# Kernel optimization log

Measured on AMD Instinct MI355X. Metric: run time of the kernel, lower is better.

The kernel has to match this reference:

```python
import jax, jax.numpy as jnp
import numpy as np

D_MODEL = 1024
NUM_HEADS = 16
D_K = D_MODEL // NUM_HEADS


def setup_inputs() -> dict:
    key = jax.random.key(0)
    ks = jax.random.split(key, 9)
    s = 1.0 / np.sqrt(D_MODEL)
    x = jax.random.normal(ks[0], (4, 2048, D_MODEL), dtype=jnp.float32)
    Wq = jax.random.uniform(ks[1], (D_MODEL, D_MODEL), jnp.float32, -s, s)
    bq = jax.random.uniform(ks[2], (D_MODEL,), jnp.float32, -s, s)
    Wk = jax.random.uniform(ks[3], (D_MODEL, D_MODEL), jnp.float32, -s, s)
    bk = jax.random.uniform(ks[4], (D_MODEL,), jnp.float32, -s, s)
    Wv = jax.random.uniform(ks[5], (D_MODEL, D_MODEL), jnp.float32, -s, s)
    bv = jax.random.uniform(ks[6], (D_MODEL,), jnp.float32, -s, s)
    Wo = jax.random.uniform(ks[7], (D_MODEL, D_MODEL), jnp.float32, -s, s)
    bo = jax.random.uniform(ks[8], (D_MODEL,), jnp.float32, -s, s)
    return {"x": x, "Wq": Wq, "bq": bq, "Wk": Wk, "bk": bk,
            "Wv": Wv, "bv": bv, "Wo": Wo, "bo": bo}


def reference(x, Wq, bq, Wk, bk, Wv, bv, Wo, bo):
    B, S, _ = x.shape
    # project and split heads: [B,S,D] -> [B,H,S,dk]
    def heads(W, b):
        return (x @ W + b).reshape(B, S, NUM_HEADS, D_K).transpose(0, 2, 1, 3)
    q = heads(Wq, bq)
    k = heads(Wk, bk)
    v = heads(Wv, bv)
    scores = jnp.einsum('bhqd,bhkd->bhqk', q, k) / jnp.sqrt(jnp.float32(D_K))
    attn = jax.nn.softmax(scores, axis=-1)
    out = jnp.einsum('bhqk,bhkd->bhqd', attn, v)
    out = out.transpose(0, 2, 1, 3).reshape(B, S, D_MODEL)
    return out @ Wo + bo
```

## Files before the change

kernel.cpp:

```cpp
#include <hip/hip_runtime.h>
#include <hip/hip_bf16.h>

#define D_MODEL 1024
#define NUM_HEADS 16
#define D_K 64
#define B_SZ 4
#define SEQ 2048
#define SCALE_Q 0.180336881f

typedef short bf16x8 __attribute__((ext_vector_type(8)));
typedef float f32x4 __attribute__((ext_vector_type(4)));
typedef unsigned short u16;

__device__ __forceinline__ unsigned cvtpk(float a, float b) {
    unsigned r;
    asm("v_cvt_pk_bf16_f32 %0, %1, %2" : "=v"(r) : "v"(a), "v"(b));
    return r;
}
__device__ __forceinline__ u16 f2bf(float f) {
    return (u16)cvtpk(f, f);
}
__device__ __forceinline__ float exp2a(float x) {
    float r;
    asm("v_exp_f32 %0, %1" : "=v"(r) : "v"(x));
    return r;
}
__device__ __forceinline__ void gload_lds16(const u16* g, u16* l) {
    __builtin_amdgcn_global_load_lds(
        (const __attribute__((address_space(1))) unsigned int*)g,
        (__attribute__((address_space(3))) unsigned int*)l, 16, 0, 0);
}

__global__ __launch_bounds__(256) void prep_all(
    const float* __restrict__ xin, u16* __restrict__ xbf,
    const float* __restrict__ W0, const float* __restrict__ W1,
    const float* __restrict__ W2, const float* __restrict__ W3,
    u16* __restrict__ Wt)
{
    __shared__ float tile[64][65];
    const int t = threadIdx.x;
    if (blockIdx.x < 1024) {
        const int n8 = (B_SZ * SEQ * D_MODEL) / 8;
        for (int i = blockIdx.x * 256 + t; i < n8; i += 1024 * 256) {
            float4 a = ((const float4*)xin)[(size_t)i * 2];
            float4 b = ((const float4*)xin)[(size_t)i * 2 + 1];
            uint4 o;
            o.x = cvtpk(a.x, a.y);
            o.y = cvtpk(a.z, a.w);
            o.z = cvtpk(b.x, b.y);
            o.w = cvtpk(b.z, b.w);
            const int j = i ^ ((i >> 7) & 7);
            ((uint4*)xbf)[j] = o;
        }
        return;
    }
    const int id = blockIdx.x - 1024;
    const int z  = id >> 8;
    const int by = (id >> 4) & 15;
    const int bx = id & 15;
    const float* W = z == 0 ? W0 : z == 1 ? W1 : z == 2 ? W2 : W3;
    u16* out = Wt + (size_t)z * D_MODEL * D_MODEL;
    const int k0 = by * 64;
    const int n0 = bx * 64;
    #pragma unroll
    for (int it = 0; it < 4; ++it) {
        int idx = it * 256 + t;
        int r = idx >> 4;
        int c = (idx & 15) * 4;
        float4 v = *(const float4*)(W + (size_t)(k0 + r) * D_MODEL + n0 + c);
        tile[r][c + 0] = v.x; tile[r][c + 1] = v.y;
        tile[r][c + 2] = v.z; tile[r][c + 3] = v.w;
    }
    __syncthreads();
    #pragma unroll
    for (int it = 0; it < 2; ++it) {
        int idx = it * 256 + t;
        int r = idx >> 3;
        int c = (idx & 7) * 8;
        uint4 o;
        o.x = cvtpk(tile[c + 0][r], tile[c + 1][r]);
        o.y = cvtpk(tile[c + 2][r], tile[c + 3][r]);
        o.z = cvtpk(tile[c + 4][r], tile[c + 5][r]);
        o.w = cvtpk(tile[c + 6][r], tile[c + 7][r]);
        const int csw = (((idx & 7) ^ (r & 7)) * 8);
        *(uint4*)(out + (size_t)(n0 + r) * D_MODEL + k0 + csw) = o;
    }
}

__global__ __launch_bounds__(512) void gemm_qkv(
    const u16* __restrict__ A, const u16* __restrict__ Wt,
    const float* __restrict__ bq, const float* __restrict__ bk,
    const float* __restrict__ bv, u16* __restrict__ Yb)
{
    __shared__ u16 As[2][128][64];
    __shared__ u16 Bs[2][128][64];
    const int t    = threadIdx.x;
    const int lane = t & 63;
    const int wid  = t >> 6;
    const int wm   = wid >> 2;
    const int wn   = wid & 3;
    const int g    = lane >> 4;
    const int lr   = lane & 15;
    const int m0   = blockIdx.y * 128;
    const int n0   = blockIdx.x * 128;
    const int K    = D_MODEL;
    const int xm   = (lr & 7) << 3;

    const int srow8 = lane >> 3;
    const int scol  = (lane & 7) * 8;

    f32x4 acc[4][2];
    #pragma unroll
    for (int i = 0; i < 4; ++i)
        #pragma unroll
        for (int j = 0; j < 2; ++j)
            acc[i][j] = (f32x4){0.f, 0.f, 0.f, 0.f};

    #pragma unroll
    for (int it = 0; it < 2; ++it) {
        const int seg = it * 8 + wid;
        gload_lds16(A  + (size_t)(m0 + seg * 8 + srow8) * K + scol, &As[0][seg * 8][0]);
        gload_lds16(Wt + (size_t)(n0 + seg * 8 + srow8) * K + scol, &Bs[0][seg * 8][0]);
    }
    __syncthreads();

    for (int k0 = 0; k0 < K; k0 += 64) {
        const int cur = (k0 >> 6) & 1;
        if (k0 + 64 < K) {
            const int nb = cur ^ 1;
            #pragma unroll
            for (int it = 0; it < 2; ++it) {
                const int seg = it * 8 + wid;
                gload_lds16(A  + (size_t)(m0 + seg * 8 + srow8) * K + k0 + 64 + scol, &As[nb][seg * 8][0]);
                gload_lds16(Wt + (size_t)(n0 + seg * 8 + srow8) * K + k0 + 64 + scol, &Bs[nb][seg * 8][0]);
            }
        }
        #pragma unroll
        for (int s = 0; s < 2; ++s) {
            bf16x8 af[4], bfr[2];
            #pragma unroll
            for (int mt = 0; mt < 4; ++mt)
                af[mt] = *(const bf16x8*)(&As[cur][wm * 64 + mt * 16 + lr][(g * 8 + s * 32) ^ xm]);
            #pragma unroll
            for (int nt = 0; nt < 2; ++nt)
                bfr[nt] = *(const bf16x8*)(&Bs[cur][wn * 32 + nt * 16 + lr][(g * 8 + s * 32) ^ xm]);
            #pragma unroll
            for (int mt = 0; mt < 4; ++mt)
                #pragma unroll
                for (int nt = 0; nt < 2; ++nt)
                    acc[mt][nt] = __builtin_amdgcn_mfma_f32_16x16x32_bf16(
                        af[mt], bfr[nt], acc[mt][nt], 0, 0, 0);
        }
        __syncthreads();
    }

    const int which = n0 >> 10;
    const float scale = (which == 0) ? SCALE_Q : 1.0f;
    const float* bp = (which == 0) ? bq : (which == 1) ? bk : bv;
    u16* dst = Yb + (size_t)which * ((size_t)B_SZ * SEQ * D_MODEL);

    float bv2[2];
    #pragma unroll
    for (int nt = 0; nt < 2; ++nt)
        bv2[nt] = bp[((n0 + wn * 32 + nt * 16 + lr) & 1023)];

    #pragma unroll
    for (int mt = 0; mt < 4; ++mt) {
        #pragma unroll
        for (int nt = 0; nt < 2; ++nt) {
            float v4[4];
            #pragma unroll
            for (int r = 0; r < 4; ++r) v4[r] = (acc[mt][nt][r] + bv2[nt]) * scale;
            const int mbase = m0 + wm * 64 + mt * 16 + g * 4;
            const int nn = (n0 + wn * 32 + nt * 16 + lr) & 1023;
            const int h = nn >> 6, d = nn & 63;
            const int bb = mbase >> 11, s2 = mbase & 2047;
            if (which == 2) {
                const int z  = s2 & 63;
                const int zp = (z & 32) + 8 * ((z & 15) >> 2) + 4 * ((z >> 4) & 1);
                const int col = zp ^ ((d & 7) << 3);
                uint2 o;
                o.x = cvtpk(v4[0], v4[1]);
                o.y = cvtpk(v4[2], v4[3]);
                *(uint2*)&dst[(((size_t)(bb * NUM_HEADS + h) * D_K + d) * SEQ) + (s2 & ~63) + col] = o;
            } else {
                #pragma unroll
                for (int r = 0; r < 4; ++r) {
                    const int s2r = s2 + r;
                    const int dd = (which == 1) ? (d ^ ((s2r & 7) << 3)) : d;
                    dst[(((size_t)(bb * NUM_HEADS + h) * SEQ) + s2r) * D_K + dd] = f2bf(v4[r]);
                }
            }
        }
    }
}

__global__ __launch_bounds__(512) void gemm_o(
    const u16* __restrict__ A, const u16* __restrict__ Wt,
    const float* __restrict__ bias, float* __restrict__ Y)
{
    __shared__ u16 As[2][128][64];
    __shared__ u16 Bs[2][128][64];
    const int t    = threadIdx.x;
    const int lane = t & 63;
    const int wid  = t >> 6;
    const int wm   = wid >> 2;
    const int wn   = wid & 3;
    const int g    = lane >> 4;
    const int lr   = lane & 15;
    const int m0   = blockIdx.y * 128;
    const int n0   = blockIdx.x * 128;
    const int K    = D_MODEL;
    const int xm   = (lr & 7) << 3;

    const int srow8 = lane >> 3;
    const int scol  = (lane & 7) * 8;

    f32x4 acc[4][2];
    #pragma unroll
    for (int i = 0; i < 4; ++i)
        #pragma unroll
        for (int j = 0; j < 2; ++j)
            acc[i][j] = (f32x4){0.f, 0.f, 0.f, 0.f};

    #pragma unroll
    for (int it = 0; it < 2; ++it) {
        const int seg = it * 8 + wid;
        gload_lds16(A  + (size_t)(m0 + seg * 8 + srow8) * K + scol, &As[0][seg * 8][0]);
        gload_lds16(Wt + (size_t)(n0 + seg * 8 + srow8) * K + scol, &Bs[0][seg * 8][0]);
    }
    __syncthreads();

    for (int k0 = 0; k0 < K; k0 += 64) {
        const int cur = (k0 >> 6) & 1;
        if (k0 + 64 < K) {
            const int nb = cur ^ 1;
            #pragma unroll
            for (int it = 0; it < 2; ++it) {
                const int seg = it * 8 + wid;
                gload_lds16(A  + (size_t)(m0 + seg * 8 + srow8) * K + k0 + 64 + scol, &As[nb][seg * 8][0]);
                gload_lds16(Wt + (size_t)(n0 + seg * 8 + srow8) * K + k0 + 64 + scol, &Bs[nb][seg * 8][0]);
            }
        }
        #pragma unroll
        for (int s = 0; s < 2; ++s) {
            bf16x8 af[4], bfr[2];
            #pragma unroll
            for (int mt = 0; mt < 4; ++mt)
                af[mt] = *(const bf16x8*)(&As[cur][wm * 64 + mt * 16 + lr][(g * 8 + s * 32) ^ xm]);
            #pragma unroll
            for (int nt = 0; nt < 2; ++nt)
                bfr[nt] = *(const bf16x8*)(&Bs[cur][wn * 32 + nt * 16 + lr][(g * 8 + s * 32) ^ xm]);
            #pragma unroll
            for (int mt = 0; mt < 4; ++mt)
                #pragma unroll
                for (int nt = 0; nt < 2; ++nt)
                    acc[mt][nt] = __builtin_amdgcn_mfma_f32_16x16x32_bf16(
                        af[mt], bfr[nt], acc[mt][nt], 0, 0, 0);
        }
        __syncthreads();
    }

    float bv2[2];
    #pragma unroll
    for (int nt = 0; nt < 2; ++nt) bv2[nt] = bias[n0 + wn * 32 + nt * 16 + lr];

    #pragma unroll
    for (int mt = 0; mt < 4; ++mt)
        #pragma unroll
        for (int nt = 0; nt < 2; ++nt)
            #pragma unroll
            for (int r = 0; r < 4; ++r) {
                const int m = m0 + wm * 64 + mt * 16 + g * 4 + r;
                const int n = n0 + wn * 32 + nt * 16 + lr;
                Y[(size_t)m * D_MODEL + n] = acc[mt][nt][r] + bv2[nt];
            }
}

__global__ __launch_bounds__(512, 4) void attn_mfma(
    const u16* __restrict__ Q, const u16* __restrict__ Kb,
    const u16* __restrict__ Vt, u16* __restrict__ ctx)
{
    __shared__ u16 Ks[2][128][64];
    __shared__ u16 Vs[2][64][128];
    const int t    = threadIdx.x;
    const int lane = t & 63;
    const int w    = t >> 6;
    const int g    = lane >> 4;
    const int lr   = lane & 15;
    const int fid  = blockIdx.x + (blockIdx.y << 3) + (blockIdx.z << 7);
    const int oid  = (fid & 7) * 64 + (fid >> 3);
    const int qt   = oid & 7;
    const int h    = (oid >> 3) & 15;
    const int b    = oid >> 7;
    const size_t hoff = ((size_t)b * NUM_HEADS + h) * SEQ * D_K;

    bf16x8 qf[2][2];
    #pragma unroll
    for (int u = 0; u < 2; ++u) {
        const int q = qt * 256 + w * 32 + u * 16 + lr;
        qf[u][0] = *(const bf16x8*)(Q + hoff + (size_t)q * D_K + g * 8);
        qf[u][1] = *(const bf16x8*)(Q + hoff + (size_t)q * D_K + g * 8 + 32);
    }

    bf16x8 onesf;
    #pragma unroll
    for (int j = 0; j < 8; ++j) onesf[j] = (short)0x3F80;

    const int krow = w * 16 + (lane >> 3);
    const int kcol = (lane & 7) * 8;
    const u16* ksrc = Kb + hoff + (size_t)krow * D_K + kcol;
    const int vrow = w * 8 + (lane >> 4);
    const int vcol = (lane & 15) * 8;
    const u16* vsrc = Vt + hoff + (size_t)vrow * SEQ + vcol;

    const int xm = (lr & 7) << 3;

    f32x4 acc_o[2][4];
    f32x4 acc_l[2];
    #pragma unroll
    for (int u = 0; u < 2; ++u) {
        acc_l[u] = (f32x4){0.f, 0.f, 0.f, 0.f};
        #pragma unroll
        for (int n = 0; n < 4; ++n) acc_o[u][n] = (f32x4){0.f, 0.f, 0.f, 0.f};
    }

    gload_lds16(ksrc,               &Ks[0][w * 16][0]);
    gload_lds16(ksrc + 8 * D_K,     &Ks[0][w * 16 + 8][0]);
    gload_lds16(vsrc,               &Vs[0][w * 8][0]);
    gload_lds16(vsrc + 4 * SEQ,     &Vs[0][w * 8 + 4][0]);

    int bu = 0;
    for (int kt = 0; kt < SEQ / 128; ++kt) {
        __syncthreads();
        if (kt + 1 < SEQ / 128) {
            const size_t kv0 = (size_t)(kt + 1) * 128;
            const int nb = bu ^ 1;
            gload_lds16(ksrc + kv0 * D_K,       &Ks[nb][w * 16][0]);
            gload_lds16(ksrc + (kv0 + 8) * D_K, &Ks[nb][w * 16 + 8][0]);
            gload_lds16(vsrc + kv0,             &Vs[nb][w * 8][0]);
            gload_lds16(vsrc + 4 * SEQ + kv0,   &Vs[nb][w * 8 + 4][0]);
        }

        #pragma unroll
        for (int hv = 0; hv < 2; ++hv) {
            f32x4 sc[2][4];
            #pragma unroll
            for (int u = 0; u < 2; ++u)
                #pragma unroll
                for (int mt = 0; mt < 4; ++mt) sc[u][mt] = (f32x4){0.f, 0.f, 0.f, 0.f};
            __builtin_amdgcn_s_setprio(1);
            #pragma unroll
            for (int s = 0; s < 2; ++s)
                #pragma unroll
                for (int mt = 0; mt < 4; ++mt) {
                    bf16x8 kf = *(const bf16x8*)(
                        &Ks[bu][hv * 64 + mt * 16 + lr][(g * 8 + s * 32) ^ xm]);
                    sc[0][mt] = __builtin_amdgcn_mfma_f32_16x16x32_bf16(kf, qf[0][s], sc[0][mt], 0, 0, 0);
                    sc[1][mt] = __builtin_amdgcn_mfma_f32_16x16x32_bf16(kf, qf[1][s], sc[1][mt], 0, 0, 0);
                }
            __builtin_amdgcn_s_setprio(0);

            union { bf16x8 v; unsigned u[4]; } pa[2][2];
            #pragma unroll
            for (int u = 0; u < 2; ++u) {
                #pragma unroll
                for (int mt = 0; mt < 4; ++mt)
                    #pragma unroll
                    for (int r = 0; r < 4; ++r)
                        sc[u][mt][r] = exp2a(sc[u][mt][r]);
                #pragma unroll
                for (int s = 0; s < 2; ++s) {
                    pa[u][s].u[0] = cvtpk(sc[u][2 * s][0],     sc[u][2 * s][1]);
                    pa[u][s].u[1] = cvtpk(sc[u][2 * s][2],     sc[u][2 * s][3]);
                    pa[u][s].u[2] = cvtpk(sc[u][2 * s + 1][0], sc[u][2 * s + 1][1]);
                    pa[u][s].u[3] = cvtpk(sc[u][2 * s + 1][2], sc[u][2 * s + 1][3]);
                }
            }

            __builtin_amdgcn_s_setprio(1);
            #pragma unroll
            for (int s = 0; s < 2; ++s) {
                #pragma unroll
                for (int n = 0; n < 4; ++n) {
                    bf16x8 vf = *(const bf16x8*)(
                        &Vs[bu][16 * n + lr][hv * 64 + ((32 * s + 8 * g) ^ xm)]);
                    acc_o[0][n] = __builtin_amdgcn_mfma_f32_16x16x32_bf16(pa[0][s].v, vf, acc_o[0][n], 0, 0, 0);
                    acc_o[1][n] = __builtin_amdgcn_mfma_f32_16x16x32_bf16(pa[1][s].v, vf, acc_o[1][n], 0, 0, 0);
                }
                acc_l[0] = __builtin_amdgcn_mfma_f32_16x16x32_bf16(pa[0][s].v, onesf, acc_l[0], 0, 0, 0);
                acc_l[1] = __builtin_amdgcn_mfma_f32_16x16x32_bf16(pa[1][s].v, onesf, acc_l[1], 0, 0, 0);
            }
            __builtin_amdgcn_s_setprio(0);
        }
        bu ^= 1;
    }

    #pragma unroll
    for (int u = 0; u < 2; ++u) {
        f32x4 linv;
        #pragma unroll
        for (int r = 0; r < 4; ++r) linv[r] = 1.0f / acc_l[u][r];
        #pragma unroll
        for (int n = 0; n < 4; ++n)
            #pragma unroll
            for (int r = 0; r < 4; ++r) {
                const int qrow = qt * 256 + w * 32 + u * 16 + 4 * g + r;
                const int col  = (h * D_K + 16 * n + lr) ^ ((qrow & 7) << 3);
                ctx[((size_t)b * SEQ + qrow) * D_MODEL + col] =
                    f2bf(acc_o[u][n][r] * linv[r]);
            }
    }
}

extern "C" void kernel_launch(void* const* d_in, const int* in_sizes, int n_in,
                              void* d_out, int out_size, void* d_ws, size_t ws_size,
                              hipStream_t stream)
{
    const float* x  = (const float*)d_in[0];
    const float* Wq = (const float*)d_in[1];
    const float* bq = (const float*)d_in[2];
    const float* Wk = (const float*)d_in[3];
    const float* bk = (const float*)d_in[4];
    const float* Wv = (const float*)d_in[5];
    const float* bv = (const float*)d_in[6];
    const float* Wo = (const float*)d_in[7];
    const float* bo = (const float*)d_in[8];
    float* out = (float*)d_out;

    char* ws = (char*)d_ws;
    const size_t MB = 1024 * 1024;
    u16* xbf  = (u16*)(ws);
    u16* Wt   = (u16*)(ws + 16 * MB);
    u16* Qbf  = (u16*)(ws + 24 * MB);
    u16* ctxb = (u16*)(ws + 72 * MB);
    u16* Kbf  = Qbf + (size_t)B_SZ * SEQ * D_MODEL;
    u16* Vtw  = Kbf + (size_t)B_SZ * SEQ * D_MODEL;

    prep_all<<<2048, 256, 0, stream>>>(x, xbf, Wq, Wk, Wv, Wo, Wt);

    gemm_qkv<<<dim3(3 * D_MODEL / 128, (B_SZ * SEQ) / 128), 512, 0, stream>>>(
        xbf, Wt, bq, bk, bv, Qbf);

    attn_mfma<<<dim3(SEQ / 256, NUM_HEADS, B_SZ), 512, 0, stream>>>(Qbf, Kbf, Vtw, ctxb);

    gemm_o<<<dim3(D_MODEL / 128, (B_SZ * SEQ) / 128), 512, 0, stream>>>(
        ctxb, Wt + 3 * (size_t)D_MODEL * D_MODEL, bo, out);
}
```

Before: 163.4 us.

## Triple-buffer GEMM K-loop with 32-wide tiles, vmcnt waits and new swizzle

New measurement: 171.2 us. 4.8% more time.

```diff
diff --git a/kernel.cpp b/kernel.cpp
--- a/kernel.cpp
+++ b/kernel.cpp
@@ -49,7 +49,7 @@
             o.y = cvtpk(a.z, a.w);
             o.z = cvtpk(b.x, b.y);
             o.w = cvtpk(b.z, b.w);
-            const int j = i ^ ((i >> 7) & 7);
+            const int j = (i & ~3) | ((i ^ (i >> 9)) & 3);
             ((uint4*)xbf)[j] = o;
         }
         return;
@@ -75,25 +75,26 @@
     #pragma unroll
     for (int it = 0; it < 2; ++it) {
         int idx = it * 256 + t;
-        int r = idx >> 3;
-        int c = (idx & 7) * 8;
+        int r  = idx >> 3;
+        int cI = idx & 7;
+        int c  = cI * 8;
         uint4 o;
         o.x = cvtpk(tile[c + 0][r], tile[c + 1][r]);
         o.y = cvtpk(tile[c + 2][r], tile[c + 3][r]);
         o.z = cvtpk(tile[c + 4][r], tile[c + 5][r]);
         o.w = cvtpk(tile[c + 6][r], tile[c + 7][r]);
-        const int csw = (((idx & 7) ^ (r & 7)) * 8);
-        *(uint4*)(out + (size_t)(n0 + r) * D_MODEL + k0 + csw) = o;
-    }
-}
-
-__global__ __launch_bounds__(512) void gemm_qkv(
+        const int cs = (cI & ~3) | ((cI ^ (r >> 2)) & 3);
+        *(uint4*)(out + (size_t)(n0 + r) * D_MODEL + k0 + cs * 8) = o;
+    }
+}
+
+__global__ __launch_bounds__(512, 4) void gemm_qkv(
     const u16* __restrict__ A, const u16* __restrict__ Wt,
     const float* __restrict__ bq, const float* __restrict__ bk,
     const float* __restrict__ bv, u16* __restrict__ Yb)
 {
-    __shared__ u16 As[2][128][64];
-    __shared__ u16 Bs[2][128][64];
+    __shared__ u16 As[3][128][32];
+    __shared__ u16 Bs[3][128][32];
     const int t    = threadIdx.x;
     const int lane = t & 63;
     const int wid  = t >> 6;
@@ -101,13 +102,13 @@
     const int wn   = wid & 3;
     const int g    = lane >> 4;
     const int lr   = lane & 15;
+    const int xc   = (lr >> 2) & 3;
     const int m0   = blockIdx.y * 128;
     const int n0   = blockIdx.x * 128;
     const int K    = D_MODEL;
-    const int xm   = (lr & 7) << 3;
-
-    const int srow8 = lane >> 3;
-    const int scol  = (lane & 7) * 8;
+
+    const u16* Asrc = A  + (size_t)(m0 + wid * 16 + (lane >> 2)) * K + (lane & 3) * 8;
+    const u16* Bsrc = Wt + (size_t)(n0 + wid * 16 + (lane >> 2)) * K + (lane & 3) * 8;
 
     f32x4 acc[4][2];
     #pragma unroll
@@ -116,42 +117,36 @@
         for (int j = 0; j < 2; ++j)
             acc[i][j] = (f32x4){0.f, 0.f, 0.f, 0.f};
 
-    #pragma unroll
-    for (int it = 0; it < 2; ++it) {
-        const int seg = it * 8 + wid;
-        gload_lds16(A  + (size_t)(m0 + seg * 8 + srow8) * K + scol, &As[0][seg * 8][0]);
-        gload_lds16(Wt + (size_t)(n0 + seg * 8 + srow8) * K + scol, &Bs[0][seg * 8][0]);
-    }
-    __syncthreads();
-
-    for (int k0 = 0; k0 < K; k0 += 64) {
-        const int cur = (k0 >> 6) & 1;
-        if (k0 + 64 < K) {
-            const int nb = cur ^ 1;
-            #pragma unroll
-            for (int it = 0; it < 2; ++it) {
-                const int seg = it * 8 + wid;
-                gload_lds16(A  + (size_t)(m0 + seg * 8 + srow8) * K + k0 + 64 + scol, &As[nb][seg * 8][0]);
-                gload_lds16(Wt + (size_t)(n0 + seg * 8 + srow8) * K + k0 + 64 + scol, &Bs[nb][seg * 8][0]);
-            }
-        }
-        #pragma unroll
-        for (int s = 0; s < 2; ++s) {
-            bf16x8 af[4], bfr[2];
-            #pragma unroll
-            for (int mt = 0; mt < 4; ++mt)
-                af[mt] = *(const bf16x8*)(&As[cur][wm * 64 + mt * 16 + lr][(g * 8 + s * 32) ^ xm]);
+    gload_lds16(Asrc,      &As[0][wid * 16][0]);
+    gload_lds16(Bsrc,      &Bs[0][wid * 16][0]);
+    gload_lds16(Asrc + 32, &As[1][wid * 16][0]);
+    gload_lds16(Bsrc + 32, &Bs[1][wid * 16][0]);
+
+    #pragma unroll
+    for (int k = 0; k < 32; ++k) {
+        if (k < 31) asm volatile("s_waitcnt vmcnt(2)" ::: "memory");
+        else        asm volatile("s_waitcnt vmcnt(0)" ::: "memory");
+        __builtin_amdgcn_s_barrier();
+        __builtin_amdgcn_sched_barrier(0);
+        if (k + 2 < 32) {
+            const int nb = (k + 2) % 3;
+            gload_lds16(Asrc + (k + 2) * 32, &As[nb][wid * 16][0]);
+            gload_lds16(Bsrc + (k + 2) * 32, &Bs[nb][wid * 16][0]);
+        }
+        const int cb = k % 3;
+        bf16x8 af[4], bfr[2];
+        #pragma unroll
+        for (int mt = 0; mt < 4; ++mt)
+            af[mt] = *(const bf16x8*)(&As[cb][wm * 64 + mt * 16 + lr][(g ^ xc) * 8]);
+        #pragma unroll
+        for (int nt = 0; nt < 2; ++nt)
+            bfr[nt] = *(const bf16x8*)(&Bs[cb][wn * 32 + nt * 16 + lr][(g ^ xc) * 8]);
+        #pragma unroll
+        for (int mt = 0; mt < 4; ++mt)
             #pragma unroll
             for (int nt = 0; nt < 2; ++nt)
-                bfr[nt] = *(const bf16x8*)(&Bs[cur][wn * 32 + nt * 16 + lr][(g * 8 + s * 32) ^ xm]);
-            #pragma unroll
-            for (int mt = 0; mt < 4; ++mt)
-                #pragma unroll
-                for (int nt = 0; nt < 2; ++nt)
-                    acc[mt][nt] = __builtin_amdgcn_mfma_f32_16x16x32_bf16(
-                        af[mt], bfr[nt], acc[mt][nt], 0, 0, 0);
-        }
-        __syncthreads();
+                acc[mt][nt] = __builtin_amdgcn_mfma_f32_16x16x32_bf16(
+                    af[mt], bfr[nt], acc[mt][nt], 0, 0, 0);
     }
 
     const int which = n0 >> 10;
@@ -195,12 +190,12 @@
     }
 }
 
-__global__ __launch_bounds__(512) void gemm_o(
+__global__ __launch_bounds__(512, 4) void gemm_o(
     const u16* __restrict__ A, const u16* __restrict__ Wt,
     const float* __restrict__ bias, float* __restrict__ Y)
 {
-    __shared__ u16 As[2][128][64];
-    __shared__ u16 Bs[2][128][64];
+    __shared__ u16 As[3][128][32];
+    __shared__ u16 Bs[3][128][32];
     const int t    = threadIdx.x;
     const int lane = t & 63;
     const int wid  = t >> 6;
@@ -208,13 +203,13 @@
     const int wn   = wid & 3;
     const int g    = lane >> 4;
     const int lr   = lane & 15;
+    const int xc   = (lr >> 2) & 3;
     const int m0   = blockIdx.y * 128;
     const int n0   = blockIdx.x * 128;
     const int K    = D_MODEL;
-    const int xm   = (lr & 7) << 3;
-
-    const int srow8 = lane >> 3;
-    const int scol  = (lane & 7) * 8;
+
+    const u16* Asrc = A  + (size_t)(m0 + wid * 16 + (lane >> 2)) * K + (lane & 3) * 8;
+    const u16* Bsrc = Wt + (size_t)(n0 + wid * 16 + (lane >> 2)) * K + (lane & 3) * 8;
 
     f32x4 acc[4][2];
     #pragma unroll
@@ -223,42 +218,36 @@
         for (int j = 0; j < 2; ++j)
             acc[i][j] = (f32x4){0.f, 0.f, 0.f, 0.f};
 
-    #pragma unroll
-    for (int it = 0; it < 2; ++it) {
-        const int seg = it * 8 + wid;
-        gload_lds16(A  + (size_t)(m0 + seg * 8 + srow8) * K + scol, &As[0][seg * 8][0]);
-        gload_lds16(Wt + (size_t)(n0 + seg * 8 + srow8) * K + scol, &Bs[0][seg * 8][0]);
-    }
-    __syncthreads();
-
-    for (int k0 = 0; k0 < K; k0 += 64) {
-        const int cur = (k0 >> 6) & 1;
-        if (k0 + 64 < K) {
-            const int nb = cur ^ 1;
-            #pragma unroll
-            for (int it = 0; it < 2; ++it) {
-                const int seg = it * 8 + wid;
-                gload_lds16(A  + (size_t)(m0 + seg * 8 + srow8) * K + k0 + 64 + scol, &As[nb][seg * 8][0]);
-                gload_lds16(Wt + (size_t)(n0 + seg * 8 + srow8) * K + k0 + 64 + scol, &Bs[nb][seg * 8][0]);
-            }
-        }
-        #pragma unroll
-        for (int s = 0; s < 2; ++s) {
-            bf16x8 af[4], bfr[2];
-            #pragma unroll
-            for (int mt = 0; mt < 4; ++mt)
-                af[mt] = *(const bf16x8*)(&As[cur][wm * 64 + mt * 16 + lr][(g * 8 + s * 32) ^ xm]);
+    gload_lds16(Asrc,      &As[0][wid * 16][0]);
+    gload_lds16(Bsrc,      &Bs[0][wid * 16][0]);
+    gload_lds16(Asrc + 32, &As[1][wid * 16][0]);
+    gload_lds16(Bsrc + 32, &Bs[1][wid * 16][0]);
+
+    #pragma unroll
+    for (int k = 0; k < 32; ++k) {
+        if (k < 31) asm volatile("s_waitcnt vmcnt(2)" ::: "memory");
+        else        asm volatile("s_waitcnt vmcnt(0)" ::: "memory");
+        __builtin_amdgcn_s_barrier();
+        __builtin_amdgcn_sched_barrier(0);
+        if (k + 2 < 32) {
+            const int nb = (k + 2) % 3;
+            gload_lds16(Asrc + (k + 2) * 32, &As[nb][wid * 16][0]);
+            gload_lds16(Bsrc + (k + 2) * 32, &Bs[nb][wid * 16][0]);
+        }
+        const int cb = k % 3;
+        bf16x8 af[4], bfr[2];
+        #pragma unroll
+        for (int mt = 0; mt < 4; ++mt)
+            af[mt] = *(const bf16x8*)(&As[cb][wm * 64 + mt * 16 + lr][(g ^ xc) * 8]);
+        #pragma unroll
+        for (int nt = 0; nt < 2; ++nt)
+            bfr[nt] = *(const bf16x8*)(&Bs[cb][wn * 32 + nt * 16 + lr][(g ^ xc) * 8]);
+        #pragma unroll
+        for (int mt = 0; mt < 4; ++mt)
             #pragma unroll
             for (int nt = 0; nt < 2; ++nt)
-                bfr[nt] = *(const bf16x8*)(&Bs[cur][wn * 32 + nt * 16 + lr][(g * 8 + s * 32) ^ xm]);
-            #pragma unroll
-            for (int mt = 0; mt < 4; ++mt)
-                #pragma unroll
-                for (int nt = 0; nt < 2; ++nt)
-                    acc[mt][nt] = __builtin_amdgcn_mfma_f32_16x16x32_bf16(
-                        af[mt], bfr[nt], acc[mt][nt], 0, 0, 0);
-        }
-        __syncthreads();
+                acc[mt][nt] = __builtin_amdgcn_mfma_f32_16x16x32_bf16(
+                    af[mt], bfr[nt], acc[mt][nt], 0, 0, 0);
     }
 
     float bv2[2];
@@ -406,8 +395,10 @@
             #pragma unroll
             for (int r = 0; r < 4; ++r) {
                 const int qrow = qt * 256 + w * 32 + u * 16 + 4 * g + r;
-                const int col  = (h * D_K + 16 * n + lr) ^ ((qrow & 7) << 3);
-                ctx[((size_t)b * SEQ + qrow) * D_MODEL + col] =
+                const int cbase = h * D_K + 16 * n + lr;
+                const int ch  = cbase >> 3;
+                const int ch2 = (ch & ~3) | ((ch ^ (qrow >> 2)) & 3);
+                ctx[((size_t)b * SEQ + qrow) * D_MODEL + (ch2 << 3) + (cbase & 7)] =
                     f2bf(acc_o[u][n][r] * linv[r]);
             }
     }
```

## Enlarge QKV GEMM tile to 256x256 with a phased ping-pong pipeline

Applied to the files above, without the earlier changes.

New measurement: 172.7 us. 1.06x slower.

```diff
diff --git a/kernel.cpp b/kernel.cpp
--- a/kernel.cpp
+++ b/kernel.cpp
@@ -87,107 +87,184 @@
     }
 }
 
-__global__ __launch_bounds__(512) void gemm_qkv(
+__global__ __launch_bounds__(512, 2) void gemm_qkv(
     const u16* __restrict__ A, const u16* __restrict__ Wt,
     const float* __restrict__ bq, const float* __restrict__ bk,
     const float* __restrict__ bv, u16* __restrict__ Yb)
 {
-    __shared__ u16 As[2][128][64];
-    __shared__ u16 Bs[2][128][64];
+    __shared__ u16 As[2][2][128][64];
+    __shared__ u16 Bs[2][2][128][64];
     const int t    = threadIdx.x;
     const int lane = t & 63;
-    const int wid  = t >> 6;
-    const int wm   = wid >> 2;
-    const int wn   = wid & 3;
-    const int g    = lane >> 4;
+    const int w    = t >> 6;
+    const int wm   = w >> 2;
+    const int wn   = w & 3;
+    const int g4   = lane >> 4;
     const int lr   = lane & 15;
-    const int m0   = blockIdx.y * 128;
-    const int n0   = blockIdx.x * 128;
+    const int xm   = (lr & 7) << 3;
+    const int m0   = blockIdx.y * 256;
+    const int n0   = blockIdx.x * 256;
     const int K    = D_MODEL;
-    const int xm   = (lr & 7) << 3;
-
-    const int srow8 = lane >> 3;
-    const int scol  = (lane & 7) * 8;
-
-    f32x4 acc[4][2];
-    #pragma unroll
-    for (int i = 0; i < 4; ++i)
-        #pragma unroll
-        for (int j = 0; j < 2; ++j)
+    const int hb   = wn >> 1;
+    const int brow = (wn & 1) * 64;
+
+    const u16* Ag = A  + (size_t)(m0 + w * 8 + (lane >> 3)) * K + (lane & 7) * 8;
+    const u16* Bg = Wt + (size_t)(n0 + w * 8 + (lane >> 3)) * K + (lane & 7) * 8;
+
+#define STAGE_A(dd, ha, tk) do {                                                   \
+        gload_lds16(Ag + (size_t)((ha) * 128) * K + (tk) * 64,                     \
+                    &As[dd][ha][w * 8][0]);                                        \
+        gload_lds16(Ag + (size_t)((ha) * 128 + 64) * K + (tk) * 64,                \
+                    &As[dd][ha][64 + w * 8][0]);                                   \
+    } while (0)
+#define STAGE_B(dd, hx, tk) do {                                                   \
+        gload_lds16(Bg + (size_t)((hx) * 128) * K + (tk) * 64,                     \
+                    &Bs[dd][hx][w * 8][0]);                                        \
+        gload_lds16(Bg + (size_t)((hx) * 128 + 64) * K + (tk) * 64,                \
+                    &Bs[dd][hx][64 + w * 8][0]);                                   \
+    } while (0)
+
+    f32x4 acc[8][4];
+    #pragma unroll
+    for (int i = 0; i < 8; ++i)
+        #pragma unroll
+        for (int j = 0; j < 4; ++j)
             acc[i][j] = (f32x4){0.f, 0.f, 0.f, 0.f};
 
-    #pragma unroll
-    for (int it = 0; it < 2; ++it) {
-        const int seg = it * 8 + wid;
-        gload_lds16(A  + (size_t)(m0 + seg * 8 + srow8) * K + scol, &As[0][seg * 8][0]);
-        gload_lds16(Wt + (size_t)(n0 + seg * 8 + srow8) * K + scol, &Bs[0][seg * 8][0]);
-    }
-    __syncthreads();
-
-    for (int k0 = 0; k0 < K; k0 += 64) {
-        const int cur = (k0 >> 6) & 1;
-        if (k0 + 64 < K) {
-            const int nb = cur ^ 1;
-            #pragma unroll
-            for (int it = 0; it < 2; ++it) {
-                const int seg = it * 8 + wid;
-                gload_lds16(A  + (size_t)(m0 + seg * 8 + srow8) * K + k0 + 64 + scol, &As[nb][seg * 8][0]);
-                gload_lds16(Wt + (size_t)(n0 + seg * 8 + srow8) * K + k0 + 64 + scol, &Bs[nb][seg * 8][0]);
-            }
-        }
-        #pragma unroll
-        for (int s = 0; s < 2; ++s) {
-            bf16x8 af[4], bfr[2];
-            #pragma unroll
-            for (int mt = 0; mt < 4; ++mt)
-                af[mt] = *(const bf16x8*)(&As[cur][wm * 64 + mt * 16 + lr][(g * 8 + s * 32) ^ xm]);
-            #pragma unroll
-            for (int nt = 0; nt < 2; ++nt)
-                bfr[nt] = *(const bf16x8*)(&Bs[cur][wn * 32 + nt * 16 + lr][(g * 8 + s * 32) ^ xm]);
-            #pragma unroll
-            for (int mt = 0; mt < 4; ++mt)
-                #pragma unroll
-                for (int nt = 0; nt < 2; ++nt)
-                    acc[mt][nt] = __builtin_amdgcn_mfma_f32_16x16x32_bf16(
-                        af[mt], bfr[nt], acc[mt][nt], 0, 0, 0);
-        }
-        __syncthreads();
-    }
+    STAGE_A(0, 0, 0); STAGE_A(0, 1, 0); STAGE_B(0, 0, 0); STAGE_B(0, 1, 0);
+    STAGE_A(1, 0, 1); STAGE_A(1, 1, 1); STAGE_B(1, 0, 1); STAGE_B(1, 1, 1);
+    asm volatile("s_waitcnt vmcnt(8)" ::: "memory");
+    __builtin_amdgcn_s_barrier();
+
+    for (int gg = 0; gg < 16; ++gg) {
+        const int d = gg & 1;
+        bf16x8 af[4][2], bf[4][2];
+
+        #pragma unroll
+        for (int j = 0; j < 4; ++j)
+            #pragma unroll
+            for (int kk = 0; kk < 2; ++kk)
+                af[j][kk] = *(const bf16x8*)(
+                    &As[d][wm][j * 16 + lr][(kk * 32 + g4 * 8) ^ xm]);
+        #pragma unroll
+        for (int nf = 0; nf < 2; ++nf)
+            #pragma unroll
+            for (int kk = 0; kk < 2; ++kk)
+                bf[nf][kk] = *(const bf16x8*)(
+                    &Bs[d][hb][brow + nf * 16 + lr][(kk * 32 + g4 * 8) ^ xm]);
+        if (gg >= 1 && gg < 15) STAGE_A(d ^ 1, 0, gg + 1);
+        __builtin_amdgcn_s_barrier();
+        asm volatile("s_waitcnt lgkmcnt(0)" ::: "memory");
+        __builtin_amdgcn_sched_barrier(0);
+        __builtin_amdgcn_s_setprio(1);
+        #pragma unroll
+        for (int j = 0; j < 4; ++j)
+            #pragma unroll
+            for (int nf = 0; nf < 2; ++nf)
+                #pragma unroll
+                for (int kk = 0; kk < 2; ++kk)
+                    acc[j][nf] = __builtin_amdgcn_mfma_f32_16x16x32_bf16(
+                        af[j][kk], bf[nf][kk], acc[j][nf], 0, 0, 0);
+        __builtin_amdgcn_s_setprio(0);
+        __builtin_amdgcn_s_barrier();
+
+        #pragma unroll
+        for (int nf = 2; nf < 4; ++nf)
+            #pragma unroll
+            for (int kk = 0; kk < 2; ++kk)
+                bf[nf][kk] = *(const bf16x8*)(
+                    &Bs[d][hb][brow + nf * 16 + lr][(kk * 32 + g4 * 8) ^ xm]);
+        if (gg >= 1 && gg < 15) STAGE_A(d ^ 1, 1, gg + 1);
+        __builtin_amdgcn_s_barrier();
+        asm volatile("s_waitcnt lgkmcnt(0)" ::: "memory");
+        __builtin_amdgcn_sched_barrier(0);
+        __builtin_amdgcn_s_setprio(1);
+        #pragma unroll
+        for (int j = 0; j < 4; ++j)
+            #pragma unroll
+            for (int nf = 2; nf < 4; ++nf)
+                #pragma unroll
+                for (int kk = 0; kk < 2; ++kk)
+                    acc[j][nf] = __builtin_amdgcn_mfma_f32_16x16x32_bf16(
+                        af[j][kk], bf[nf][kk], acc[j][nf], 0, 0, 0);
+        __builtin_amdgcn_s_setprio(0);
+        __builtin_amdgcn_s_barrier();
+
+        #pragma unroll
+        for (int j = 0; j < 4; ++j)
+            #pragma unroll
+            for (int kk = 0; kk < 2; ++kk)
+                af[j][kk] = *(const bf16x8*)(
+                    &As[d][wm][64 + j * 16 + lr][(kk * 32 + g4 * 8) ^ xm]);
+        if (gg < 14) STAGE_B(d, 0, gg + 2);
+        __builtin_amdgcn_s_barrier();
+        asm volatile("s_waitcnt lgkmcnt(0)" ::: "memory");
+        __builtin_amdgcn_sched_barrier(0);
+        __builtin_amdgcn_s_setprio(1);
+        #pragma unroll
+        for (int j = 0; j < 4; ++j)
+            #pragma unroll
+            for (int nf = 2; nf < 4; ++nf)
+                #pragma unroll
+                for (int kk = 0; kk < 2; ++kk)
+                    acc[4 + j][nf] = __builtin_amdgcn_mfma_f32_16x16x32_bf16(
+                        af[j][kk], bf[nf][kk], acc[4 + j][nf], 0, 0, 0);
+        __builtin_amdgcn_s_setprio(0);
+        __builtin_amdgcn_s_barrier();
+
+        if (gg < 14) STAGE_B(d, 1, gg + 2);
+        __builtin_amdgcn_s_barrier();
+        __builtin_amdgcn_s_setprio(1);
+        #pragma unroll
+        for (int j = 0; j < 4; ++j)
+            #pragma unroll
+            for (int nf = 0; nf < 2; ++nf)
+                #pragma unroll
+                for (int kk = 0; kk < 2; ++kk)
+                    acc[4 + j][nf] = __builtin_amdgcn_mfma_f32_16x16x32_bf16(
+                        af[j][kk], bf[nf][kk], acc[4 + j][nf], 0, 0, 0);
+        __builtin_amdgcn_s_setprio(0);
+        if (gg <= 13)      asm volatile("s_waitcnt vmcnt(4)" ::: "memory");
+        else if (gg == 14) asm volatile("s_waitcnt vmcnt(0)" ::: "memory");
+        __builtin_amdgcn_s_barrier();
+    }
+#undef STAGE_A
+#undef STAGE_B
 
     const int which = n0 >> 10;
     const float scale = (which == 0) ? SCALE_Q : 1.0f;
     const float* bp = (which == 0) ? bq : (which == 1) ? bk : bv;
     u16* dst = Yb + (size_t)which * ((size_t)B_SZ * SEQ * D_MODEL);
 
-    float bv2[2];
-    #pragma unroll
-    for (int nt = 0; nt < 2; ++nt)
-        bv2[nt] = bp[((n0 + wn * 32 + nt * 16 + lr) & 1023)];
-
-    #pragma unroll
-    for (int mt = 0; mt < 4; ++mt) {
-        #pragma unroll
-        for (int nt = 0; nt < 2; ++nt) {
+    float bv4[4];
+    #pragma unroll
+    for (int nf = 0; nf < 4; ++nf)
+        bv4[nf] = bp[((n0 + wn * 64 + nf * 16 + lr) & 1023)];
+
+    #pragma unroll
+    for (int mf = 0; mf < 8; ++mf) {
+        #pragma unroll
+        for (int nf = 0; nf < 4; ++nf) {
             float v4[4];
             #pragma unroll
-            for (int r = 0; r < 4; ++r) v4[r] = (acc[mt][nt][r] + bv2[nt]) * scale;
-            const int mbase = m0 + wm * 64 + mt * 16 + g * 4;
-            const int nn = (n0 + wn * 32 + nt * 16 + lr) & 1023;
-            const int h = nn >> 6, d = nn & 63;
+            for (int r = 0; r < 4; ++r) v4[r] = (acc[mf][nf][r] + bv4[nf]) * scale;
+            const int mbase = m0 + wm * 128 + mf * 16 + g4 * 4;
+            const int nn = (n0 + wn * 64 + nf * 16 + lr) & 1023;
+            const int h = nn >> 6, dcol = nn & 63;
             const int bb = mbase >> 11, s2 = mbase & 2047;
             if (which == 2) {
                 const int z  = s2 & 63;
                 const int zp = (z & 32) + 8 * ((z & 15) >> 2) + 4 * ((z >> 4) & 1);
-                const int col = zp ^ ((d & 7) << 3);
+                const int col = zp ^ ((dcol & 7) << 3);
                 uint2 o;
                 o.x = cvtpk(v4[0], v4[1]);
                 o.y = cvtpk(v4[2], v4[3]);
-                *(uint2*)&dst[(((size_t)(bb * NUM_HEADS + h) * D_K + d) * SEQ) + (s2 & ~63) + col] = o;
+                *(uint2*)&dst[(((size_t)(bb * NUM_HEADS + h) * D_K + dcol) * SEQ) + (s2 & ~63) + col] = o;
             } else {
                 #pragma unroll
                 for (int r = 0; r < 4; ++r) {
                     const int s2r = s2 + r;
-                    const int dd = (which == 1) ? (d ^ ((s2r & 7) << 3)) : d;
+                    const int dd = (which == 1) ? (dcol ^ ((s2r & 7) << 3)) : dcol;
                     dst[(((size_t)(bb * NUM_HEADS + h) * SEQ) + s2r) * D_K + dd] = f2bf(v4[r]);
                 }
             }
@@ -439,7 +516,7 @@
 
     prep_all<<<2048, 256, 0, stream>>>(x, xbf, Wq, Wk, Wv, Wo, Wt);
 
-    gemm_qkv<<<dim3(3 * D_MODEL / 128, (B_SZ * SEQ) / 128), 512, 0, stream>>>(
+    gemm_qkv<<<dim3(3 * D_MODEL / 256, (B_SZ * SEQ) / 256), 512, 0, stream>>>(
         xbf, Wt, bq, bk, bv, Qbf);
 
     attn_mfma<<<dim3(SEQ / 256, NUM_HEADS, B_SZ), 512, 0, stream>>>(Qbf, Kbf, Vtw, ctxb);
```
